# Performance work log

Measured on AMD Instinct MI355X. Metric: run time of the kernel, lower is better.

## Reference

```python
import jax, jax.numpy as jnp
import numpy as np

P, B, H, IN, L = 64, 256, 512, 2, 2


def setup_inputs() -> dict:
    key = jax.random.key(0)
    ks = jax.random.split(key, 16)
    s = 1.0 / np.sqrt(H)
    inp = {
        'input_traces': jax.random.normal(ks[0], (B, P, IN), jnp.float32),
        'h0': jax.random.normal(ks[1], (P, L, B, H), jnp.float32) * 0.1,
        'c0': jax.random.normal(ks[2], (P, L, B, H), jnp.float32) * 0.1,
        # layer 0 LSTM params (PyTorch layout: [4H, in] with gate order i,f,g,o)
        'w_ih0': jax.random.uniform(ks[3], (4 * H, IN), jnp.float32, -s, s),
        'w_hh0': jax.random.uniform(ks[4], (4 * H, H), jnp.float32, -s, s),
        'b_ih0': jax.random.uniform(ks[5], (4 * H,), jnp.float32, -s, s),
        'b_hh0': jax.random.uniform(ks[6], (4 * H,), jnp.float32, -s, s),
        # layer 1 LSTM params
        'w_ih1': jax.random.uniform(ks[7], (4 * H, H), jnp.float32, -s, s),
        'w_hh1': jax.random.uniform(ks[8], (4 * H, H), jnp.float32, -s, s),
        'b_ih1': jax.random.uniform(ks[9], (4 * H,), jnp.float32, -s, s),
        'b_hh1': jax.random.uniform(ks[10], (4 * H,), jnp.float32, -s, s),
    }
    return inp


def _lstm_forward(input_traces, h0, c0, params):
    # Fuse pedestrian and batch dims into one big batch PB = P*B; the original
    # loops over pedestrians calling the SAME LSTM weights, so this is exact.
    x = jnp.transpose(input_traces, (1, 0, 2)).reshape(P * B, IN)  # [PB, 2]
    h = jnp.transpose(h0, (1, 0, 2, 3)).reshape(L, P * B, H)       # [L, PB, H]
    c = jnp.transpose(c0, (1, 0, 2, 3)).reshape(L, P * B, H)
    h_next, c_next = [], []
    for l in range(L):
        wi, wh, bi, bh = params[l]
        gates = x @ wi.T + bi + h[l] @ wh.T + bh                   # [PB, 4H]
        ig, fg, gg, og = jnp.split(gates, 4, axis=-1)
        ig, fg, og = jax.nn.sigmoid(ig), jax.nn.sigmoid(fg), jax.nn.sigmoid(og)
        gg = jnp.tanh(gg)
        c_new = fg * c[l] + ig * gg
        h_new = og * jnp.tanh(c_new)
        h_next.append(h_new)
        c_next.append(c_new)
        x = h_new
    out = x.reshape(P, B, H).transpose(1, 0, 2)                    # [B, P, H]
    hn = jnp.stack(h_next).reshape(L, P, B, H).transpose(1, 0, 2, 3)
    cn = jnp.stack(c_next).reshape(L, P, B, H).transpose(1, 0, 2, 3)
    return out, hn, cn


def reference(input_traces, h0, c0, w_ih0, w_hh0, b_ih0, b_hh0,
              w_ih1, w_hh1, b_ih1, b_hh1):
    params = [(w_ih0, w_hh0, b_ih0, b_hh0), (w_ih1, w_hh1, b_ih1, b_hh1)]
    return _lstm_forward(input_traces, h0, c0, params)
```

## Files before the change

kernel.cpp:

```cpp
#include <hip/hip_runtime.h>
#include <hip/hip_bf16.h>

#define PP 64
#define BB 256
#define HH 512
#define MM (PP * BB)

#define HN_BASE (BB * PP * HH)
#define CN_BASE (HN_BASE + PP * 2 * BB * HH)

#define TILE_BYTES 16384
#define WS_A0   0ull
#define WS_A1A  16777216ull
#define WS_A1B  33554432ull
#define WS_W0   50331648ull
#define WS_W1A  52428800ull
#define WS_W1B  54525952ull
#define WS_NEED 56623104ull

typedef __attribute__((ext_vector_type(8))) short bf16x8;
typedef __attribute__((ext_vector_type(4))) float floatx4;

__device__ __forceinline__ float sigf(float x) { return 1.0f / (1.0f + __expf(-x)); }
__device__ __forceinline__ float tanh_(float x) { return 2.0f / (1.0f + __expf(-2.0f * x)) - 1.0f; }

__device__ __forceinline__ short f2bf(float f) {
  unsigned u = __float_as_uint(f);
  u = (u + 0x7FFFu + ((u >> 16) & 1u)) >> 16;
  return (short)u;
}

template <typename T>
__device__ __forceinline__ float tofl(T v);
template <> __device__ __forceinline__ float tofl<float>(float v) { return v; }
template <> __device__ __forceinline__ float tofl<__hip_bfloat16>(__hip_bfloat16 v) { return __bfloat162float(v); }

template <typename T>
__device__ __forceinline__ T fromfl(float v);
template <> __device__ __forceinline__ float fromfl<float>(float v) { return v; }
template <> __device__ __forceinline__ __hip_bfloat16 fromfl<__hip_bfloat16>(float v) { return __float2bfloat16(v); }

template <typename T>
__device__ __forceinline__ bf16x8 load8(const T* p);
template <> __device__ __forceinline__ bf16x8 load8<__hip_bfloat16>(const __hip_bfloat16* p) {
  return *(const bf16x8*)p;
}
template <> __device__ __forceinline__ bf16x8 load8<float>(const float* p) {
  float4 f0 = *(const float4*)p;
  float4 f1 = *((const float4*)p + 1);
  bf16x8 v;
  v[0] = f2bf(f0.x); v[1] = f2bf(f0.y); v[2] = f2bf(f0.z); v[3] = f2bf(f0.w);
  v[4] = f2bf(f1.x); v[5] = f2bf(f1.y); v[6] = f2bf(f1.z); v[7] = f2bf(f1.w);
  return v;
}

__device__ __forceinline__ bool detect_f32(const void* w_ih0) {
  const unsigned short* p = (const unsigned short*)w_ih0;
  int l = threadIdx.x & 63;
  unsigned short a = p[2 * l], b = p[2 * l + 1];
  int big = ((a & 0x7F80) >= 0x3F80) || ((b & 0x7F80) >= 0x3F80);
  return __any(big);
}

__device__ __forceinline__ void gload16(void* ldsp, const void* g) {
  __builtin_amdgcn_global_load_lds(
      (const __attribute__((address_space(1))) unsigned int*)g,
      (__attribute__((address_space(3))) unsigned int*)ldsp, 16, 0, 0);
}


template <typename T>
__device__ __forceinline__ void prep_A_body(const T* __restrict__ h0, char* __restrict__ ws) {
  const int pb = blockIdx.x, kt = blockIdx.y, l = blockIdx.z;
  char* dst = ws + (l ? WS_A1B : WS_A0) + ((size_t)(pb * 8 + kt)) * TILE_BYTES;
  const int ped = pb >> 1, bh = pb & 1;
  const T* src = h0 + ((size_t)(ped * 2 + l) * 256) * 512;
  const int tid = threadIdx.x;
#pragma unroll
  for (int i = 0; i < 4; ++i) {
    int idx = i * 256 + tid;
    int ln  = idx & 63;
    int ks  = (idx >> 6) & 1;
    int rb  = idx >> 7;
    int row = bh * 128 + rb * 16 + (ln & 15);
    int col = kt * 64 + ks * 32 + (ln >> 4) * 8;
    *(bf16x8*)(dst + (size_t)idx * 16) = load8<T>(src + (size_t)row * 512 + col);
  }
}

__global__ void __launch_bounds__(256) prep_A_k(const void* h0, const void* det, void* ws) {
  if (detect_f32(det)) prep_A_body<float>((const float*)h0, (char*)ws);
  else prep_A_body<__hip_bfloat16>((const __hip_bfloat16*)h0, (char*)ws);
}

template <typename T>
__device__ __forceinline__ void prep_W_body(const T* __restrict__ w0, const T* __restrict__ w1a,
                                            const T* __restrict__ w1b, char* __restrict__ ws) {
  const int m = blockIdx.x >> 4, hb = blockIdx.x & 15, kt = blockIdx.y;
  const T* src = (m == 0) ? w0 : (m == 1 ? w1a : w1b);
  const size_t base = (m == 0) ? WS_W0 : (m == 1 ? WS_W1A : WS_W1B);
  char* dst = ws + base + ((size_t)(hb * 8 + kt)) * TILE_BYTES;
  const int tid = threadIdx.x;
#pragma unroll
  for (int i = 0; i < 4; ++i) {
    int idx = i * 256 + tid;
    int ln  = idx & 63;
    int ks  = (idx >> 6) & 1;
    int rb  = idx >> 7;
    int g   = rb >> 1, half = rb & 1;
    int j   = g * 512 + hb * 32 + half * 16 + (ln & 15);
    int col = kt * 64 + ks * 32 + (ln >> 4) * 8;
    *(bf16x8*)(dst + (size_t)idx * 16) = load8<T>(src + (size_t)j * 512 + col);
  }
}

__global__ void __launch_bounds__(256) prep_W_k(const void* w0, const void* w1a, const void* w1b,
                                                const void* det, void* ws) {
  if (detect_f32(det)) prep_W_body<float>((const float*)w0, (const float*)w1a, (const float*)w1b, (char*)ws);
  else prep_W_body<__hip_bfloat16>((const __hip_bfloat16*)w0, (const __hip_bfloat16*)w1a,
                                   (const __hip_bfloat16*)w1b, (char*)ws);
}

template <typename T, int LAYER>
__device__ __forceinline__ void lstm_dma_body(
    const T* __restrict__ xin, const T* __restrict__ c0,
    const T* __restrict__ wih, const T* __restrict__ bih, const T* __restrict__ bhh,
    T* __restrict__ out, char* __restrict__ ws, char* lds)
{
  const int tid  = threadIdx.x;
  const int nb   = blockIdx.x;
  const int hb   = blockIdx.y;
  const int lane = tid & 63;
  const int wid  = tid >> 6;
  const int quad = lane >> 4;
  const int lrow = lane & 15;
  const int p0   = nb >> 1;

  floatx4 acc[4][4];
#pragma unroll
  for (int g = 0; g < 4; ++g)
#pragma unroll
    for (int mi = 0; mi < 4; ++mi)
#pragma unroll
      for (int q = 0; q < 4; ++q) acc[g][mi][q] = 0.0f;

  const int a_rb0  = (wid >> 1) * 4;
  const int w_half = wid & 1;

  constexpr int KITERS = (LAYER == 0) ? 8 : 16;

  auto stage = [&](int buf, int kt) {
    const char *at, *wt;
    if (LAYER == 0) {
      at = ws + WS_A0  + ((size_t)(nb * 8 + kt)) * TILE_BYTES;
      wt = ws + WS_W0  + ((size_t)(hb * 8 + kt)) * TILE_BYTES;
    } else if (kt < 8) {
      at = ws + WS_A1A + ((size_t)(nb * 8 + kt)) * TILE_BYTES;
      wt = ws + WS_W1A + ((size_t)(hb * 8 + kt)) * TILE_BYTES;
    } else {
      at = ws + WS_A1B + ((size_t)(nb * 8 + kt - 8)) * TILE_BYTES;
      wt = ws + WS_W1B + ((size_t)(hb * 8 + kt - 8)) * TILE_BYTES;
    }
    char* la = lds + buf * 32768;
    char* lw = la + TILE_BYTES;
#pragma unroll
    for (int i = 0; i < 4; ++i) {
      int base = (i * 4 + wid) * 1024;
      int off  = base + lane * 16;
      gload16(la + base, at + off);
      gload16(lw + base, wt + off);
    }
  };

  stage(0, 0);
  __syncthreads();

#pragma unroll
  for (int kt = 0; kt < KITERS; ++kt) {
    const int cur = kt & 1;
    if (kt + 1 < KITERS) stage(cur ^ 1, kt + 1);

    const char* la = lds + cur * 32768;
    const char* lw = la + TILE_BYTES;
#pragma unroll
    for (int ks = 0; ks < 2; ++ks) {
      bf16x8 aF[4], wF[4];
#pragma unroll
      for (int mi = 0; mi < 4; ++mi)
        aF[mi] = *(const bf16x8*)(la + (((a_rb0 + mi) * 2 + ks) * 1024) + lane * 16);
#pragma unroll
      for (int g = 0; g < 4; ++g)
        wF[g] = *(const bf16x8*)(lw + (((g * 2 + w_half) * 2 + ks) * 1024) + lane * 16);
#pragma unroll
      for (int g = 0; g < 4; ++g)
#pragma unroll
        for (int mi = 0; mi < 4; ++mi)
          acc[g][mi] = __builtin_amdgcn_mfma_f32_16x16x32_bf16(
              aF[mi], wF[g], acc[g][mi], 0, 0, 0);
    }
    __syncthreads();
  }

  const int hloc = hb * 32 + w_half * 16 + lrow;
  float bias[4], wx0[4], wx1[4];
#pragma unroll
  for (int g = 0; g < 4; ++g) {
    int j = g * 512 + hloc;
    bias[g] = tofl<T>(bih[j]) + tofl<T>(bhh[j]);
    if (LAYER == 0) {
      wx0[g] = tofl<T>(wih[j * 2]);
      wx1[g] = tofl<T>(wih[j * 2 + 1]);
    }
  }
  const int crow0 = (p0 * 2 + LAYER) * 256;
  const int kt_h = hloc >> 6;
  const int ks_h = (hloc >> 5) & 1;
  const int qd_h = (hloc >> 3) & 3;
  const int el_h = hloc & 7;
  char* a1a_tile = ws + WS_A1A + ((size_t)(nb * 8 + kt_h)) * TILE_BYTES;

#pragma unroll
  for (int mi = 0; mi < 4; ++mi) {
#pragma unroll
    for (int r = 0; r < 4; ++r) {
      int rr = (wid >> 1) * 64 + mi * 16 + quad * 4 + r;
      int b  = ((nb & 1) << 7) + rr;
      float gv0 = acc[0][mi][r] + bias[0];
      float gv1 = acc[1][mi][r] + bias[1];
      float gv2 = acc[2][mi][r] + bias[2];
      float gv3 = acc[3][mi][r] + bias[3];
      if (LAYER == 0) {
        float x0 = tofl<T>(xin[(b * 64 + p0) * 2]);
        float x1 = tofl<T>(xin[(b * 64 + p0) * 2 + 1]);
        gv0 += x0 * wx0[0] + x1 * wx1[0];
        gv1 += x0 * wx0[1] + x1 * wx1[1];
        gv2 += x0 * wx0[2] + x1 * wx1[2];
        gv3 += x0 * wx0[3] + x1 * wx1[3];
      }
      float ig = sigf(gv0), fg = sigf(gv1);
      float gg = tanh_(gv2), og = sigf(gv3);
      size_t ro = ((size_t)(crow0 + b)) * 512 + hloc;
      float co   = tofl<T>(c0[ro]);
      float cnew = fg * co + ig * gg;
      float hnew = og * tanh_(cnew);
      out[HN_BASE + ro] = fromfl<T>(hnew);
      out[CN_BASE + ro] = fromfl<T>(cnew);
      if (LAYER == 0) {
        int slot = (((rr >> 4) * 2 + ks_h) * 64) + qd_h * 16 + (rr & 15);
        *(short*)(a1a_tile + (size_t)slot * 16 + el_h * 2) = f2bf(hnew);
      }
      if (LAYER == 1)
        out[(size_t)(b * 64 + p0) * 512 + hloc] = fromfl<T>(hnew);
    }
  }
}

template <int LAYER>
__global__ void __launch_bounds__(256)
lstm_dma(const void* xin, const void* c0, const void* wih,
         const void* bih, const void* bhh, const void* det,
         void* out, void* ws)
{
  __shared__ __align__(16) char lds[2 * 32768];
  if (detect_f32(det)) {
    lstm_dma_body<float, LAYER>((const float*)xin, (const float*)c0, (const float*)wih,
                                (const float*)bih, (const float*)bhh,
                                (float*)out, (char*)ws, lds);
  } else {
    lstm_dma_body<__hip_bfloat16, LAYER>((const __hip_bfloat16*)xin, (const __hip_bfloat16*)c0,
                                         (const __hip_bfloat16*)wih, (const __hip_bfloat16*)bih,
                                         (const __hip_bfloat16*)bhh,
                                         (__hip_bfloat16*)out, (char*)ws, lds);
  }
}

template <typename T, int LAYER>
__device__ __forceinline__ void lstm_body(
    const T* __restrict__ xin, const T* __restrict__ h0, const T* __restrict__ c0,
    const T* __restrict__ wih, const T* __restrict__ whh,
    const T* __restrict__ bih, const T* __restrict__ bhh,
    T* out, __hip_bfloat16* ldsA, __hip_bfloat16* ldsW)
{
  const int tid  = threadIdx.x;
  const int nb   = blockIdx.x;
  const int hb   = blockIdx.y;
  const int lane = tid & 63;
  const int wid  = tid >> 6;
  const int quad = lane >> 4;
  const int lrow = lane & 15;
  const int p0   = nb >> 1;

  floatx4 acc[4][4];
#pragma unroll
  for (int g = 0; g < 4; ++g)
#pragma unroll
    for (int mi = 0; mi < 4; ++mi)
#pragma unroll
      for (int q = 0; q < 4; ++q) acc[g][mi][q] = 0.0f;

  int arow[4], wrow[4];
#pragma unroll
  for (int mi = 0; mi < 4; ++mi) arow[mi] = (wid >> 1) * 64 + mi * 16 + lrow;
#pragma unroll
  for (int g = 0; g < 4; ++g) wrow[g] = g * 32 + (wid & 1) * 16 + lrow;

  const int sr = tid >> 3;
  const int sc = tid & 7;
  const int KITERS = (LAYER == 0) ? 8 : 16;

  for (int kt = 0; kt < KITERS; ++kt) {
    bf16x8 ra[4], rw[4];
#pragma unroll
    for (int round = 0; round < 4; ++round) {
      int r = sr + round * 32;
      int b = ((nb & 1) << 7) + r;
      const T* srcA;
      if (LAYER == 0) {
        srcA = h0 + ((size_t)((p0 * 2) * 256 + b)) * 512 + kt * 64 + sc * 8;
      } else {
        if (kt < 8)
          srcA = out + HN_BASE + ((size_t)((p0 * 2) * 256 + b)) * 512 + kt * 64 + sc * 8;
        else
          srcA = h0 + ((size_t)((p0 * 2 + 1) * 256 + b)) * 512 + (kt - 8) * 64 + sc * 8;
      }
      ra[round] = load8<T>(srcA);

      int j = (r >> 5) * 512 + hb * 32 + (r & 31);
      const T* srcW;
      if (LAYER == 0) {
        srcW = whh + (size_t)j * 512 + kt * 64 + sc * 8;
      } else {
        if (kt < 8) srcW = wih + (size_t)j * 512 + kt * 64 + sc * 8;
        else        srcW = whh + (size_t)j * 512 + (kt - 8) * 64 + sc * 8;
      }
      rw[round] = load8<T>(srcW);
    }

    __syncthreads();
#pragma unroll
    for (int round = 0; round < 4; ++round) {
      int r = sr + round * 32;
      int p = sc ^ (r & 7);
      *(bf16x8*)((char*)ldsA + r * 128 + p * 16) = ra[round];
      *(bf16x8*)((char*)ldsW + r * 128 + p * 16) = rw[round];
    }
    __syncthreads();

#pragma unroll
    for (int ks = 0; ks < 2; ++ks) {
      bf16x8 aF[4], wF[4];
#pragma unroll
      for (int mi = 0; mi < 4; ++mi) {
        int ch = (ks * 4 + quad) ^ (arow[mi] & 7);
        aF[mi] = *(const bf16x8*)((const char*)ldsA + arow[mi] * 128 + ch * 16);
      }
#pragma unroll
      for (int g = 0; g < 4; ++g) {
        int ch = (ks * 4 + quad) ^ (wrow[g] & 7);
        wF[g] = *(const bf16x8*)((const char*)ldsW + wrow[g] * 128 + ch * 16);
      }
#pragma unroll
      for (int g = 0; g < 4; ++g)
#pragma unroll
        for (int mi = 0; mi < 4; ++mi)
          acc[g][mi] = __builtin_amdgcn_mfma_f32_16x16x32_bf16(
              aF[mi], wF[g], acc[g][mi], 0, 0, 0);
    }
  }

  const int hloc = hb * 32 + (wid & 1) * 16 + lrow;
  float bias[4], wx0[4], wx1[4];
#pragma unroll
  for (int g = 0; g < 4; ++g) {
    int j = g * 512 + hloc;
    bias[g] = tofl<T>(bih[j]) + tofl<T>(bhh[j]);
    if (LAYER == 0) {
      wx0[g] = tofl<T>(wih[j * 2]);
      wx1[g] = tofl<T>(wih[j * 2 + 1]);
    }
  }
  const int crow0 = (p0 * 2 + LAYER) * 256;
#pragma unroll
  for (int mi = 0; mi < 4; ++mi) {
#pragma unroll
    for (int r = 0; r < 4; ++r) {
      int b = ((nb & 1) << 7) + (wid >> 1) * 64 + mi * 16 + quad * 4 + r;
      float gv0 = acc[0][mi][r] + bias[0];
      float gv1 = acc[1][mi][r] + bias[1];
      float gv2 = acc[2][mi][r] + bias[2];
      float gv3 = acc[3][mi][r] + bias[3];
      if (LAYER == 0) {
        float x0 = tofl<T>(xin[(b * 64 + p0) * 2]);
        float x1 = tofl<T>(xin[(b * 64 + p0) * 2 + 1]);
        gv0 += x0 * wx0[0] + x1 * wx1[0];
        gv1 += x0 * wx0[1] + x1 * wx1[1];
        gv2 += x0 * wx0[2] + x1 * wx1[2];
        gv3 += x0 * wx0[3] + x1 * wx1[3];
      }
      float ig = sigf(gv0), fg = sigf(gv1);
      float gg = tanh_(gv2), og = sigf(gv3);
      size_t ro = ((size_t)(crow0 + b)) * 512 + hloc;
      float co   = tofl<T>(c0[ro]);
      float cnew = fg * co + ig * gg;
      float hnew = og * tanh_(cnew);
      out[HN_BASE + ro] = fromfl<T>(hnew);
      out[CN_BASE + ro] = fromfl<T>(cnew);
      if (LAYER == 1)
        out[(size_t)(b * 64 + p0) * 512 + hloc] = fromfl<T>(hnew);
    }
  }
}

template <int LAYER>
__global__ void __launch_bounds__(256)
lstm_layer(const void* xin, const void* h0, const void* c0,
           const void* wih, const void* whh, const void* bih, const void* bhh,
           const void* w_ih0_detect, void* out)
{
  __shared__ __align__(16) __hip_bfloat16 ldsA[128 * 64];
  __shared__ __align__(16) __hip_bfloat16 ldsW[128 * 64];
  if (detect_f32(w_ih0_detect)) {
    lstm_body<float, LAYER>((const float*)xin, (const float*)h0, (const float*)c0,
                            (const float*)wih, (const float*)whh,
                            (const float*)bih, (const float*)bhh,
                            (float*)out, ldsA, ldsW);
  } else {
    lstm_body<__hip_bfloat16, LAYER>((const __hip_bfloat16*)xin, (const __hip_bfloat16*)h0,
                                     (const __hip_bfloat16*)c0, (const __hip_bfloat16*)wih,
                                     (const __hip_bfloat16*)whh, (const __hip_bfloat16*)bih,
                                     (const __hip_bfloat16*)bhh, (__hip_bfloat16*)out,
                                     ldsA, ldsW);
  }
}

extern "C" void kernel_launch(void* const* d_in, const int* in_sizes, int n_in,
                              void* d_out, int out_size, void* d_ws, size_t ws_size,
                              hipStream_t stream) {
  dim3 block(256);
  if (d_ws != nullptr && ws_size >= WS_NEED) {
    prep_A_k<<<dim3(128, 8, 2), block, 0, stream>>>(d_in[1], d_in[3], d_ws);
    prep_W_k<<<dim3(48, 8), block, 0, stream>>>(d_in[4], d_in[7], d_in[8], d_in[3], d_ws);
    dim3 grid(MM / 128, HH / 32);
    lstm_dma<0><<<grid, block, 0, stream>>>(d_in[0], d_in[2], d_in[3],
                                            d_in[5], d_in[6], d_in[3], d_out, d_ws);
    lstm_dma<1><<<grid, block, 0, stream>>>(d_in[0], d_in[2], d_in[3],
                                            d_in[9], d_in[10], d_in[3], d_out, d_ws);
  } else {
    dim3 grid(MM / 128, HH / 32);
    lstm_layer<0><<<grid, block, 0, stream>>>(d_in[0], d_in[1], d_in[2],
                                              d_in[3], d_in[4], d_in[5], d_in[6],
                                              d_in[3], d_out);
    lstm_layer<1><<<grid, block, 0, stream>>>(d_in[0], d_in[1], d_in[2],
                                              d_in[7], d_in[8], d_in[9], d_in[10],
                                              d_in[3], d_out);
  }
}
```

Baseline: 496.4 us.

## Halve K-tile to 32, shrink LDS, swap grid order for occupancy

Shrinks the pre-packed K tile from 64 to 32 columns (8 KB per operand tile), halving LDS per block to 32 KB and doubling the K-loop iterations. It adds a launch-bounds hint of 4 blocks per CU and swaps grid dimensions so blocks sharing an A tile (same nb) run adjacently across hb. The aim is higher occupancy and better L2 reuse of the activation tiles. The cost is twice as many barriers per output tile and less MFMA work between syncs.

```diff
diff --git a/kernel.cpp b/kernel.cpp
--- a/kernel.cpp
+++ b/kernel.cpp
@@ -9,7 +9,7 @@
 #define HN_BASE (BB * PP * HH)
 #define CN_BASE (HN_BASE + PP * 2 * BB * HH)
 
-#define TILE_BYTES 16384
+#define TILE8K 8192
 #define WS_A0   0ull
 #define WS_A1A  16777216ull
 #define WS_A1B  33554432ull
@@ -72,18 +72,17 @@
 template <typename T>
 __device__ __forceinline__ void prep_A_body(const T* __restrict__ h0, char* __restrict__ ws) {
   const int pb = blockIdx.x, kt = blockIdx.y, l = blockIdx.z;
-  char* dst = ws + (l ? WS_A1B : WS_A0) + ((size_t)(pb * 8 + kt)) * TILE_BYTES;
+  char* dst = ws + (l ? WS_A1B : WS_A0) + ((size_t)(pb * 16 + kt)) * TILE8K;
   const int ped = pb >> 1, bh = pb & 1;
   const T* src = h0 + ((size_t)(ped * 2 + l) * 256) * 512;
   const int tid = threadIdx.x;
 #pragma unroll
-  for (int i = 0; i < 4; ++i) {
+  for (int i = 0; i < 2; ++i) {
     int idx = i * 256 + tid;
     int ln  = idx & 63;
-    int ks  = (idx >> 6) & 1;
-    int rb  = idx >> 7;
+    int rb  = idx >> 6;
     int row = bh * 128 + rb * 16 + (ln & 15);
-    int col = kt * 64 + ks * 32 + (ln >> 4) * 8;
+    int col = kt * 32 + (ln >> 4) * 8;
     *(bf16x8*)(dst + (size_t)idx * 16) = load8<T>(src + (size_t)row * 512 + col);
   }
 }
@@ -99,17 +98,16 @@
   const int m = blockIdx.x >> 4, hb = blockIdx.x & 15, kt = blockIdx.y;
   const T* src = (m == 0) ? w0 : (m == 1 ? w1a : w1b);
   const size_t base = (m == 0) ? WS_W0 : (m == 1 ? WS_W1A : WS_W1B);
-  char* dst = ws + base + ((size_t)(hb * 8 + kt)) * TILE_BYTES;
+  char* dst = ws + base + ((size_t)(hb * 16 + kt)) * TILE8K;
   const int tid = threadIdx.x;
 #pragma unroll
-  for (int i = 0; i < 4; ++i) {
+  for (int i = 0; i < 2; ++i) {
     int idx = i * 256 + tid;
     int ln  = idx & 63;
-    int ks  = (idx >> 6) & 1;
-    int rb  = idx >> 7;
+    int rb  = idx >> 6;
     int g   = rb >> 1, half = rb & 1;
     int j   = g * 512 + hb * 32 + half * 16 + (ln & 15);
-    int col = kt * 64 + ks * 32 + (ln >> 4) * 8;
+    int col = kt * 32 + (ln >> 4) * 8;
     *(bf16x8*)(dst + (size_t)idx * 16) = load8<T>(src + (size_t)j * 512 + col);
   }
 }
@@ -128,8 +126,8 @@
     T* __restrict__ out, char* __restrict__ ws, char* lds)
 {
   const int tid  = threadIdx.x;
-  const int nb   = blockIdx.x;
-  const int hb   = blockIdx.y;
+  const int hb   = blockIdx.x;
+  const int nb   = blockIdx.y;
   const int lane = tid & 63;
   const int wid  = tid >> 6;
   const int quad = lane >> 4;
@@ -147,24 +145,24 @@
   const int a_rb0  = (wid >> 1) * 4;
   const int w_half = wid & 1;
 
-  constexpr int KITERS = (LAYER == 0) ? 8 : 16;
+  constexpr int KITERS = (LAYER == 0) ? 16 : 32;
 
   auto stage = [&](int buf, int kt) {
     const char *at, *wt;
     if (LAYER == 0) {
-      at = ws + WS_A0  + ((size_t)(nb * 8 + kt)) * TILE_BYTES;
-      wt = ws + WS_W0  + ((size_t)(hb * 8 + kt)) * TILE_BYTES;
-    } else if (kt < 8) {
-      at = ws + WS_A1A + ((size_t)(nb * 8 + kt)) * TILE_BYTES;
-      wt = ws + WS_W1A + ((size_t)(hb * 8 + kt)) * TILE_BYTES;
+      at = ws + WS_A0  + ((size_t)(nb * 16 + kt)) * TILE8K;
+      wt = ws + WS_W0  + ((size_t)(hb * 16 + kt)) * TILE8K;
+    } else if (kt < 16) {
+      at = ws + WS_A1A + ((size_t)(nb * 16 + kt)) * TILE8K;
+      wt = ws + WS_W1A + ((size_t)(hb * 16 + kt)) * TILE8K;
     } else {
-      at = ws + WS_A1B + ((size_t)(nb * 8 + kt - 8)) * TILE_BYTES;
-      wt = ws + WS_W1B + ((size_t)(hb * 8 + kt - 8)) * TILE_BYTES;
-    }
-    char* la = lds + buf * 32768;
-    char* lw = la + TILE_BYTES;
-#pragma unroll
-    for (int i = 0; i < 4; ++i) {
+      at = ws + WS_A1B + ((size_t)(nb * 16 + kt - 16)) * TILE8K;
+      wt = ws + WS_W1B + ((size_t)(hb * 16 + kt - 16)) * TILE8K;
+    }
+    char* la = lds + buf * 16384;
+    char* lw = la + TILE8K;
+#pragma unroll
+    for (int i = 0; i < 2; ++i) {
       int base = (i * 4 + wid) * 1024;
       int off  = base + lane * 16;
       gload16(la + base, at + off);
@@ -180,24 +178,22 @@
     const int cur = kt & 1;
     if (kt + 1 < KITERS) stage(cur ^ 1, kt + 1);
 
-    const char* la = lds + cur * 32768;
-    const char* lw = la + TILE_BYTES;
-#pragma unroll
-    for (int ks = 0; ks < 2; ++ks) {
-      bf16x8 aF[4], wF[4];
+    const char* la = lds + cur * 16384;
+    const char* lw = la + TILE8K;
+    bf16x8 aF[4], wF[4];
+#pragma unroll
+    for (int mi = 0; mi < 4; ++mi)
+      aF[mi] = *(const bf16x8*)(la + ((a_rb0 + mi) * 1024) + lane * 16);
+#pragma unroll
+    for (int g = 0; g < 4; ++g)
+      wF[g] = *(const bf16x8*)(lw + ((g * 2 + w_half) * 1024) + lane * 16);
+#pragma unroll
+    for (int g = 0; g < 4; ++g)
 #pragma unroll
       for (int mi = 0; mi < 4; ++mi)
-        aF[mi] = *(const bf16x8*)(la + (((a_rb0 + mi) * 2 + ks) * 1024) + lane * 16);
-#pragma unroll
-      for (int g = 0; g < 4; ++g)
-        wF[g] = *(const bf16x8*)(lw + (((g * 2 + w_half) * 2 + ks) * 1024) + lane * 16);
-#pragma unroll
-      for (int g = 0; g < 4; ++g)
-#pragma unroll
-        for (int mi = 0; mi < 4; ++mi)
-          acc[g][mi] = __builtin_amdgcn_mfma_f32_16x16x32_bf16(
-              aF[mi], wF[g], acc[g][mi], 0, 0, 0);
-    }
+        acc[g][mi] = __builtin_amdgcn_mfma_f32_16x16x32_bf16(
+            aF[mi], wF[g], acc[g][mi], 0, 0, 0);
+
     __syncthreads();
   }
 
@@ -213,11 +209,10 @@
     }
   }
   const int crow0 = (p0 * 2 + LAYER) * 256;
-  const int kt_h = hloc >> 6;
-  const int ks_h = (hloc >> 5) & 1;
+  const int kt_h = hloc >> 5;
   const int qd_h = (hloc >> 3) & 3;
   const int el_h = hloc & 7;
-  char* a1a_tile = ws + WS_A1A + ((size_t)(nb * 8 + kt_h)) * TILE_BYTES;
+  char* a1a_tile = ws + WS_A1A + ((size_t)(nb * 16 + kt_h)) * TILE8K;
 
 #pragma unroll
   for (int mi = 0; mi < 4; ++mi) {
@@ -246,7 +241,7 @@
       out[HN_BASE + ro] = fromfl<T>(hnew);
       out[CN_BASE + ro] = fromfl<T>(cnew);
       if (LAYER == 0) {
-        int slot = (((rr >> 4) * 2 + ks_h) * 64) + qd_h * 16 + (rr & 15);
+        int slot = ((rr >> 4) * 64) + qd_h * 16 + (rr & 15);
         *(short*)(a1a_tile + (size_t)slot * 16 + el_h * 2) = f2bf(hnew);
       }
       if (LAYER == 1)
@@ -256,12 +251,12 @@
 }
 
 template <int LAYER>
-__global__ void __launch_bounds__(256)
+__global__ void __launch_bounds__(256, 4)
 lstm_dma(const void* xin, const void* c0, const void* wih,
          const void* bih, const void* bhh, const void* det,
          void* out, void* ws)
 {
-  __shared__ __align__(16) char lds[2 * 32768];
+  __shared__ __align__(16) char lds[2 * 16384];
   if (detect_f32(det)) {
     lstm_dma_body<float, LAYER>((const float*)xin, (const float*)c0, (const float*)wih,
                                 (const float*)bih, (const float*)bhh,
@@ -438,9 +433,9 @@
                               hipStream_t stream) {
   dim3 block(256);
   if (d_ws != nullptr && ws_size >= WS_NEED) {
-    prep_A_k<<<dim3(128, 8, 2), block, 0, stream>>>(d_in[1], d_in[3], d_ws);
-    prep_W_k<<<dim3(48, 8), block, 0, stream>>>(d_in[4], d_in[7], d_in[8], d_in[3], d_ws);
-    dim3 grid(MM / 128, HH / 32);
+    prep_A_k<<<dim3(128, 16, 2), block, 0, stream>>>(d_in[1], d_in[3], d_ws);
+    prep_W_k<<<dim3(48, 16), block, 0, stream>>>(d_in[4], d_in[7], d_in[8], d_in[3], d_ws);
+    dim3 grid(HH / 32, MM / 128);
     lstm_dma<0><<<grid, block, 0, stream>>>(d_in[0], d_in[2], d_in[3],
                                             d_in[5], d_in[6], d_in[3], d_out, d_ws);
     lstm_dma<1><<<grid, block, 0, stream>>>(d_in[0], d_in[2], d_in[3],
```

New measurement: 457.7 us. 1.08x faster.
